# Kernel tuning notes

Hardware: AMD Instinct MI355X
Metric: run time of the kernel (lower is better)

Reference implementation:

```python
import jax, jax.numpy as jnp
from jax import lax
import numpy as np

HID = 150     # FFNN hidden dim
EMB = 300     # GloVe dim (input_dim)
LSTM = 200    # lstm_dim -> state_dim = 400
T = 768       # tokens in doc
VOCAB = 50000


def _ffnn(x, W1, b1, W2, b2, W3, b3):
    h = jax.nn.relu(x @ W1.T + b1)
    h = jax.nn.relu(h @ W2.T + b2)
    return h @ W3.T + b3


def _lstm_dir(x, Wih, Whh, b):
    H = Whh.shape[1]
    def step(carry, xt):
        h, c = carry
        z = xt @ Wih.T + h @ Whh.T + b
        i, f, g, o = jnp.split(z, 4, axis=-1)
        c = jax.nn.sigmoid(f) * c + jax.nn.sigmoid(i) * jnp.tanh(g)
        h = jax.nn.sigmoid(o) * jnp.tanh(c)
        return (h, c), h
    init = (jnp.zeros((H,), x.dtype), jnp.zeros((H,), x.dtype))
    _, hs = lax.scan(step, init, x)
    return hs


def setup_inputs():
    key = jax.random.key(0)
    ks = iter(jax.random.split(key, 40))
    def w(shape, s=0.05):
        return jax.random.normal(next(ks), shape, jnp.float32) * s
    state = 2 * LSTM
    span = 2 * state + EMB + 1   # 1101
    pair = 3 * span              # 3303
    z = lambda n: jnp.zeros((n,), jnp.float32)
    return {
        'tokens': jax.random.randint(next(ks), (T,), 0, VOCAB),
        'emb': w((VOCAB, EMB), 0.3),
        'Wih_f': w((4 * LSTM, EMB)), 'Whh_f': w((4 * LSTM, LSTM)), 'b_f': z(4 * LSTM),
        'Wih_b': w((4 * LSTM, EMB)), 'Whh_b': w((4 * LSTM, LSTM)), 'b_b': z(4 * LSTM),
        'aW1': w((HID, state)), 'ab1': z(HID), 'aW2': w((HID, HID)), 'ab2': z(HID), 'aW3': w((1, HID)), 'ab3': z(1),
        'sW1': w((HID, span)), 'sb1': z(HID), 'sW2': w((HID, HID)), 'sb2': z(HID), 'sW3': w((1, HID)), 'sb3': z(1),
        'pW1': w((HID, pair)), 'pb1': z(HID), 'pW2': w((HID, HID)), 'pb2': z(HID), 'pW3': w((1, HID)), 'pb3': z(1),
    }


def reference(tokens, emb, Wih_f, Whh_f, b_f, Wih_b, Whh_b, b_b,
              aW1, ab1, aW2, ab2, aW3, ab3,
              sW1, sb1, sW2, sb2, sW3, sb3,
              pW1, pb1, pW2, pb2, pW3, pb3):
    Tn = tokens.shape[0]
    x = emb[tokens]  # (T, 300) frozen GloVe embeds
    h = jnp.concatenate([_lstm_dir(x, Wih_f, Whh_f, b_f),
                         _lstm_dir(x[::-1], Wih_b, Whh_b, b_b)[::-1]], axis=-1)  # (T, 400)
    # dropout omitted (eval mode / identity)
    attn_logits = _ffnn(h, aW1, ab1, aW2, ab2, aW3, ab3)[:, 0]  # per-token attn score (T,)
    gs, i1s, i2s = [], [], []
    for n in range(1, 11):  # span widths 1..10
        starts = jnp.arange(Tn - n + 1)
        idx = starts[:, None] + jnp.arange(n)[None, :]           # (S_n, n)
        wgt = jax.nn.softmax(attn_logits[idx], axis=-1)          # per-span softmax over LSTM-state scores
        pooled = jnp.einsum('sn,snd->sd', wgt, x[idx])           # attention pools raw embeds (as original)
        g = jnp.concatenate([h[starts], h[starts + n - 1], pooled,
                             jnp.full((Tn - n + 1, 1), float(n), jnp.float32)], axis=-1)
        gs.append(g); i1s.append(starts); i2s.append(starts + n - 1)
    g = jnp.concatenate(gs, 0)                                    # (S, 1101)
    i1 = jnp.concatenate(i1s, 0); i2 = jnp.concatenate(i2s, 0)
    S = g.shape[0]
    sm = _ffnn(g, sW1, sb1, sW2, sb2, sW3, sb3)[:, 0]             # span scores (S,)
    order = jnp.argsort(-sm)                                      # stable desc sort, as Python sorted(reverse=True)
    i1o, i2o = i1[order], i2[order]
    # greedy overlap filter: keep span if fully taken OR both endpoints free; mark taken only when kept
    def body(k, carry):
        taken, keep = carry
        a, b = i1o[k], i2o[k]
        offs = jnp.clip(a + jnp.arange(10), 0, Tn - 1)
        valid = (a + jnp.arange(10)) <= b
        all_taken = jnp.all(jnp.where(valid, taken[offs], True))
        ok = all_taken | (~taken[a] & ~taken[b])
        keep = keep.at[k].set(ok)
        taken = taken.at[offs].max(valid & ok)
        return (taken, keep)
    _, keep = lax.fori_loop(0, S, body, (jnp.zeros((Tn,), bool), jnp.zeros((S,), bool)))
    K = int(round(Tn * 0.4))
    rank = jnp.cumsum(keep.astype(jnp.int32))
    pos = jnp.where(keep & (rank <= K), rank - 1, S)
    sel = jnp.argsort(pos)[:K]            # first K kept spans, score order (>=T width-1 spans always kept)
    sel = sel[jnp.argsort(i1o[sel])]      # stable sort by span start
    g_f = g[order][sel]; sm_f = sm[order][sel]
    i1_f = i1o[sel]; i2_f = i2o[sel]
    ii, jj = np.tril_indices(K, -1)       # row-major == nested (i, j<i) loop order
    pairs = jnp.concatenate([g_f[ii], g_f[jj], g_f[ii] * g_f[jj]], axis=-1)  # (P, 3303)
    sa = _ffnn(pairs, pW1, pb1, pW2, pb2, pW3, pb3)[:, 0]
    # sij[i, j] = sm_i + sm_j + sa_ij for j < i; diag/upper = 0 (the epsilon antecedent)
    sij = jnp.zeros((K, K), jnp.float32).at[ii, jj].set(sm_f[ii] + sm_f[jj] + sa)
    return sij, i1_f, i2_f
```

## Files before the change

### kernel.cpp

```cpp
#include <hip/hip_runtime.h>
#include <math.h>
#include <float.h>

#define TN      768
#define EMBD    300
#define XPAD    304
#define LSTMD   200
#define G4      800
#define STATE   400
#define HIDD    150
#define NPADC   160
#define SPAND   1101
#define KP      1120
#define NSPANS  7635
#define NSEL    307
#define SORTN   8192

typedef unsigned long long ull;

#define OFF_X       0u
#define OFF_ZXF     233472u
#define OFF_ZXB     847872u
#define OFF_H       1462272u
#define OFF_ATTN    1769472u
#define OFF_I1      1770496u
#define OFF_I2      1778176u
#define OFF_SM      1785856u
#define OFF_SELK    1793536u
#define OFF_SELSPAN 1794048u
#define OFF_SMF     1794560u
#define OFF_A       1795072u
#define OFF_B       1844224u
#define OFF_WTF     1893376u
#define OFF_WTB     2133376u
#define OFF_AW1T    2373376u
#define OFF_AW2T    2437376u
#define OFF_SW1T    2461376u
#define OFF_SW2T    2640576u
#define OFF_PW1AT   2664576u
#define OFF_PW1BT   2843776u
#define OFF_PW1CT   3022976u
#define OFF_PW2T    3202176u
#define OFF_G       3226176u

#define REP50(M) M(0) M(1) M(2) M(3) M(4) M(5) M(6) M(7) M(8) M(9) \
 M(10) M(11) M(12) M(13) M(14) M(15) M(16) M(17) M(18) M(19) \
 M(20) M(21) M(22) M(23) M(24) M(25) M(26) M(27) M(28) M(29) \
 M(30) M(31) M(32) M(33) M(34) M(35) M(36) M(37) M(38) M(39) \
 M(40) M(41) M(42) M(43) M(44) M(45) M(46) M(47) M(48) M(49)

__device__ __forceinline__ float sigf(float x) { return 1.f / (1.f + __expf(-x)); }
__device__ __forceinline__ float tanhf_(float x) {
    x = fminf(15.f, fmaxf(-15.f, x));
    float e = __expf(2.f * x);
    return (e - 1.f) / (e + 1.f);
}

__global__ void k_gather(const int* __restrict__ tokens, const float* __restrict__ emb,
                         float* __restrict__ x) {
    int t = blockIdx.x;
    int tok = tokens[t];
    for (int d = threadIdx.x; d < XPAD; d += 256)
        x[t * XPAD + d] = (d < EMBD) ? emb[(size_t)tok * EMBD + d] : 0.f;
}

__global__ void k_transpose(const float* __restrict__ src, float* __restrict__ dst,
                            int N, int K, int srcStride, int colOff, int Npad) {
    int k = blockIdx.x;
    int n = blockIdx.y * 256 + threadIdx.x;
    if (n >= Npad) return;
    float v = 0.f;
    if (k < K && n < N) v = src[(size_t)n * srcStride + colOff + k];
    dst[(size_t)k * Npad + n] = v;
}

__global__ void k_zx(const float* __restrict__ x, const float* __restrict__ WTf,
                     const float* __restrict__ WTb, const float* __restrict__ bf,
                     const float* __restrict__ bb, float* __restrict__ zxf,
                     float* __restrict__ zxb) {
    __shared__ float xl[8 * XPAD];
    int tid = threadIdx.x;
    int bm = blockIdx.x, dir = blockIdx.y;
    for (int l = tid; l < 8 * XPAD; l += 256) xl[l] = x[(size_t)(bm * 8) * XPAD + l];
    __syncthreads();
    const float* WT = dir ? WTb : WTf;
    const float* bv = dir ? bb : bf;
    float* zx = dir ? zxb : zxf;
    for (int jj = 0; jj < 4; ++jj) {
        int n = tid + 256 * jj;
        if (n >= G4) break;
        float acc[8] = {0, 0, 0, 0, 0, 0, 0, 0};
        for (int k = 0; k < EMBD; ++k) {
            float wv = WT[(size_t)k * G4 + n];
#pragma unroll
            for (int r = 0; r < 8; ++r) acc[r] = fmaf(xl[r * XPAD + k], wv, acc[r]);
        }
        float bias = bv[n];
#pragma unroll
        for (int r = 0; r < 8; ++r) {
            int row = bm * 8 + r;
            int trow = dir ? (TN - 1 - row) : row;
            zx[(size_t)trow * G4 + n] = acc[r] + bias;
        }
    }
}

__global__ __launch_bounds__(256, 1) void k_lstm_mb(const float* __restrict__ zxf,
                                                    const float* __restrict__ zxb,
                                                    const float* __restrict__ Whh_f,
                                                    const float* __restrict__ Whh_b,
                                                    float* __restrict__ hcat,
                                                    ull* __restrict__ hq) {
    int blk = blockIdx.x;
    int dir = blk >> 2, b = blk & 3;
    const float* zx = dir ? zxb : zxf;
    const float* Whh = dir ? Whh_b : Whh_f;
    ull* hqd = hq + (size_t)dir * TN * 256;
    int tid = threadIdx.x;
    __shared__ __align__(16) float hprev[LSTMD];
    __shared__ float zl[200];
    bool active = tid < 200;
    int q = tid / 50, u = tid % 50;
    int gr = q * 200 + b * 50 + u;
    int grs = active ? gr : 0;
    const float4* wr = (const float4*)(Whh + (size_t)grs * LSTMD);
#define WDECL(i) float4 w##i = wr[i];
    REP50(WDECL)
#undef WDECL
    float c = 0.f;
    for (int l = tid; l < LSTMD; l += 256) hprev[l] = 0.f;
    int remote_idx = (tid < b * 50) ? tid : tid + 50;
    __syncthreads();
    float zpre = zx[grs];
    for (int t = 0; t < TN; ++t) {
        float acc = zpre;
        const float4* h4 = (const float4*)hprev;
#define WFMA(i) { float4 hv = h4[i]; \
        acc = fmaf(w##i.x, hv.x, acc); acc = fmaf(w##i.y, hv.y, acc); \
        acc = fmaf(w##i.z, hv.z, acc); acc = fmaf(w##i.w, hv.w, acc); }
        REP50(WFMA)
#undef WFMA
        if (active) zl[tid] = acc;
        __syncthreads();
        int trow = dir ? (TN - 1 - t) : t;
        if (tid < 50) {
            float zi = zl[tid], zf = zl[50 + tid], zg = zl[100 + tid], zo = zl[150 + tid];
            c = sigf(zf) * c + sigf(zi) * tanhf_(zg);
            float h = sigf(zo) * tanhf_(c);
            hcat[(size_t)trow * STATE + dir * LSTMD + b * 50 + tid] = h;
            hprev[b * 50 + tid] = h;
            if (t + 1 < TN) {
                ull pk = (ull)__float_as_uint(h) | ((ull)(unsigned)(t + 1) << 32);
                __hip_atomic_store(&hqd[(size_t)t * 256 + b * 50 + tid], pk,
                                   __ATOMIC_RELAXED, __HIP_MEMORY_SCOPE_AGENT);
            }
        }
        if (t + 1 < TN) {
            zpre = zx[(size_t)(t + 1) * G4 + grs];
            if (tid < 150) {
                const ull* p = &hqd[(size_t)t * 256 + remote_idx];
                ull v;
                do {
                    v = __hip_atomic_load(p, __ATOMIC_RELAXED, __HIP_MEMORY_SCOPE_AGENT);
                } while ((unsigned)(v >> 32) != (unsigned)(t + 1));
                hprev[remote_idx] = __uint_as_float((unsigned)v);
            }
            __syncthreads();
        }
    }
}

__global__ void k_attn(const float* __restrict__ hcat, const float* __restrict__ aW1T,
                       const float* __restrict__ ab1, const float* __restrict__ aW2T,
                       const float* __restrict__ ab2, const float* __restrict__ aW3,
                       const float* __restrict__ ab3, float* __restrict__ attn) {
    __shared__ float hrow[STATE];
    __shared__ float l1[NPADC];
    __shared__ float l2[NPADC];
    __shared__ float red[256];
    int t = blockIdx.x, tid = threadIdx.x;
    for (int d = tid; d < STATE; d += 256) hrow[d] = hcat[(size_t)t * STATE + d];
    __syncthreads();
    if (tid < HIDD) {
        float acc = ab1[tid];
        for (int k = 0; k < STATE; ++k) acc = fmaf(hrow[k], aW1T[(size_t)k * NPADC + tid], acc);
        l1[tid] = fmaxf(acc, 0.f);
    }
    __syncthreads();
    if (tid < HIDD) {
        float acc = ab2[tid];
        for (int k = 0; k < HIDD; ++k) acc = fmaf(l1[k], aW2T[(size_t)k * NPADC + tid], acc);
        l2[tid] = fmaxf(acc, 0.f);
    }
    __syncthreads();
    float partial = (tid < HIDD) ? l2[tid] * aW3[tid] : 0.f;
    red[tid] = partial;
    __syncthreads();
    for (int s = 128; s > 0; s >>= 1) {
        if (tid < s) red[tid] += red[tid + s];
        __syncthreads();
    }
    if (tid == 0) attn[t] = red[0] + ab3[0];
}

__global__ void k_spans(const float* __restrict__ attn, const float* __restrict__ hcat,
                        const float* __restrict__ x, float* __restrict__ g,
                        int* __restrict__ i1s, int* __restrict__ i2s) {
    int s = blockIdx.x;
    int n = 1, base = 0;
    while (s >= base + (TN - n + 1)) { base += TN - n + 1; n++; }
    int a = s - base, b = a + n - 1;
    int lane = threadIdx.x;
    float e[10];
    float mx = -FLT_MAX;
#pragma unroll
    for (int k = 0; k < 10; ++k)
        if (k < n) { e[k] = attn[a + k]; mx = fmaxf(mx, e[k]); }
    float ssum = 0.f;
#pragma unroll
    for (int k = 0; k < 10; ++k)
        if (k < n) { e[k] = __expf(e[k] - mx); ssum += e[k]; }
    float w[10];
#pragma unroll
    for (int k = 0; k < 10; ++k) w[k] = (k < n) ? e[k] / ssum : 0.f;

    float* grow = g + (size_t)s * KP;
    for (int d = lane; d < STATE; d += 64) grow[d] = hcat[(size_t)a * STATE + d];
    for (int d = lane; d < STATE; d += 64) grow[STATE + d] = hcat[(size_t)b * STATE + d];
    for (int d = lane; d < EMBD; d += 64) {
        float p = 0.f;
#pragma unroll
        for (int k = 0; k < 10; ++k)
            if (k < n) p = fmaf(w[k], x[(size_t)(a + k) * XPAD + d], p);
        grow[2 * STATE + d] = p;
    }
    if (lane == 0) { grow[1100] = (float)n; i1s[s] = a; i2s[s] = b; }
    for (int d = SPAND + lane; d < KP; d += 64) grow[d] = 0.f;
}

__global__ void k_sm(const float* __restrict__ g, const float* __restrict__ sW1T,
                     const float* __restrict__ sb1, const float* __restrict__ sW2T,
                     const float* __restrict__ sb2, const float* __restrict__ sW3,
                     const float* __restrict__ sb3, float* __restrict__ smo) {
    __shared__ float As[32 * 33];
    __shared__ float Bs[32 * NPADC];
    __shared__ float L1[32 * 161];
    int tid = threadIdx.x;
    int tx = tid & 31, ty = tid >> 5;
    int row0 = blockIdx.x * 32;
    float acc[4][5] = {};
    for (int kb = 0; kb < KP; kb += 32) {
        for (int l = tid; l < 32 * 32; l += 256) {
            int r = l >> 5, cc = l & 31;
            int gr = row0 + r;
            As[r * 33 + cc] = (gr < NSPANS) ? g[(size_t)gr * KP + kb + cc] : 0.f;
        }
        for (int l = tid; l < 32 * NPADC; l += 256) {
            int r = l / NPADC, cc = l - NPADC * r;
            Bs[l] = sW1T[(size_t)(kb + r) * NPADC + cc];
        }
        __syncthreads();
        for (int kk = 0; kk < 32; ++kk) {
            float bv[5];
#pragma unroll
            for (int jn = 0; jn < 5; ++jn) bv[jn] = Bs[kk * NPADC + tx + 32 * jn];
#pragma unroll
            for (int i4 = 0; i4 < 4; ++i4) {
                float av = As[(ty * 4 + i4) * 33 + kk];
#pragma unroll
                for (int jn = 0; jn < 5; ++jn) acc[i4][jn] = fmaf(av, bv[jn], acc[i4][jn]);
            }
        }
        __syncthreads();
    }
#pragma unroll
    for (int i4 = 0; i4 < 4; ++i4)
#pragma unroll
        for (int jn = 0; jn < 5; ++jn) {
            int nn = tx + 32 * jn;
            float v = acc[i4][jn] + (nn < HIDD ? sb1[nn] : 0.f);
            L1[(ty * 4 + i4) * 161 + nn] = fmaxf(v, 0.f);
        }
    __syncthreads();
    float acc2[4][5] = {};
    for (int kk = 0; kk < HIDD; ++kk) {
        float bv[5];
#pragma unroll
        for (int jn = 0; jn < 5; ++jn) bv[jn] = sW2T[(size_t)kk * NPADC + tx + 32 * jn];
#pragma unroll
        for (int i4 = 0; i4 < 4; ++i4) {
            float av = L1[(ty * 4 + i4) * 161 + kk];
#pragma unroll
            for (int jn = 0; jn < 5; ++jn) acc2[i4][jn] = fmaf(av, bv[jn], acc2[i4][jn]);
        }
    }
    float part[4];
#pragma unroll
    for (int i4 = 0; i4 < 4; ++i4) {
        float p = 0.f;
#pragma unroll
        for (int jn = 0; jn < 5; ++jn) {
            int nn = tx + 32 * jn;
            float v = acc2[i4][jn] + (nn < HIDD ? sb2[nn] : 0.f);
            v = fmaxf(v, 0.f);
            p = fmaf(v, (nn < HIDD ? sW3[nn] : 0.f), p);
        }
        part[i4] = p;
    }
    for (int s = 16; s > 0; s >>= 1)
#pragma unroll
        for (int i4 = 0; i4 < 4; ++i4) part[i4] += __shfl_xor(part[i4], s, 32);
    if (tx == 0)
#pragma unroll
        for (int i4 = 0; i4 < 4; ++i4) {
            int gr = row0 + ty * 4 + i4;
            if (gr < NSPANS) smo[gr] = part[i4] + sb3[0];
        }
}

__global__ __launch_bounds__(1024) void k_sortsel(const float* __restrict__ sm,
                                                  const int* __restrict__ i1s,
                                                  const int* __restrict__ i2s,
                                                  int* __restrict__ selk,
                                                  int* __restrict__ selspan,
                                                  float* __restrict__ smf,
                                                  float* __restrict__ out) {
    __shared__ float ks[SORTN];
    __shared__ unsigned short id16[SORTN];
    __shared__ int ka2[512];
    __shared__ int va2[512];
    int tid = threadIdx.x;
    for (int i = tid; i < SORTN; i += 1024) {
        ks[i] = (i < NSPANS) ? sm[i] : -FLT_MAX;
        id16[i] = (unsigned short)i;
    }
    __syncthreads();
    for (int size = 2; size <= SORTN; size <<= 1) {
        for (int stride = size >> 1; stride > 0; stride >>= 1) {
            for (int t = tid; t < SORTN / 2; t += 1024) {
                int i = ((t & ~(stride - 1)) << 1) | (t & (stride - 1));
                int j = i + stride;
                float ki = ks[i], kj = ks[j];
                unsigned short ai = id16[i], aj = id16[j];
                bool less_ji = (kj > ki) || (kj == ki && aj < ai);
                bool asc = ((i & size) == 0);
                if (less_ji == asc) {
                    ks[i] = kj; ks[j] = ki;
                    id16[i] = aj; id16[j] = ai;
                }
            }
            __syncthreads();
        }
    }
    unsigned* abu = reinterpret_cast<unsigned*>(ks);
    for (int k = tid; k < NSPANS; k += 1024) {
        int sid = id16[k];
        abu[k] = (unsigned)i1s[sid] | ((unsigned)i2s[sid] << 16);
    }
    __syncthreads();
    if (tid < 64) {
        int l = tid;
        unsigned tk = 0;
        int cnt = 0;
        for (int k = 0; k < NSPANS && cnt < NSEL; ++k) {
            unsigned ab = abu[k];
            int a = (int)(ab & 0xFFFFu), b = (int)(ab >> 16);
            int lo = a - (l << 5), hi = b - (l << 5);
            lo = lo < 0 ? 0 : lo;
            hi = hi > 31 ? 31 : hi;
            unsigned m = 0;
            if (hi >= lo) {
                unsigned upper = (hi == 31) ? 0xFFFFFFFFu : ((1u << (hi + 1)) - 1u);
                m = upper & ~((1u << lo) - 1u);
            }
            bool cov = ((tk & m) == m);
            bool all_taken = __all((int)cov);
            int la = a >> 5, lb = b >> 5;
            unsigned long long bal_a = __ballot((int)((l == la) && ((tk >> (a & 31)) & 1u)));
            unsigned long long bal_b = __ballot((int)((l == lb) && ((tk >> (b & 31)) & 1u)));
            bool ok = all_taken || (bal_a == 0ull && bal_b == 0ull);
            if (ok) {
                tk |= m;
                if (l == 0) selk[cnt] = k;
                cnt++;
            }
        }
    }
    __syncthreads();
    if (tid < 512) {
        int r = tid;
        int key = 0x7FFFFFFF;
        if (r < NSEL) {
            int k = selk[r];
            int a = (int)(abu[k] & 0xFFFFu);
            key = (a << 9) | r;
        }
        ka2[r] = key;
        va2[r] = r;
    }
    __syncthreads();
    for (int size = 2; size <= 512; size <<= 1) {
        for (int stride = size >> 1; stride > 0; stride >>= 1) {
            if (tid < 256) {
                int t = tid;
                int i = ((t & ~(stride - 1)) << 1) | (t & (stride - 1));
                int j = i + stride;
                int ki = ka2[i], kj = ka2[j];
                bool asc = ((i & size) == 0);
                if ((kj < ki) == asc) {
                    ka2[i] = kj; ka2[j] = ki;
                    int vi = va2[i]; va2[i] = va2[j]; va2[j] = vi;
                }
            }
            __syncthreads();
        }
    }
    if (tid < NSEL) {
        int r = va2[tid];
        int k = selk[r];
        int sid = id16[k];
        unsigned ab = abu[k];
        selspan[tid] = sid;
        smf[tid] = sm[sid];
        out[NSEL * NSEL + tid] = (float)(ab & 0xFFFFu);
        out[NSEL * NSEL + NSEL + tid] = (float)(ab >> 16);
    }
}

__global__ void k_AB(const float* __restrict__ g, const int* __restrict__ selspan,
                     const float* __restrict__ pW1aT, const float* __restrict__ pW1bT,
                     const float* __restrict__ pb1, float* __restrict__ Aw,
                     float* __restrict__ Bw) {
    __shared__ float grow[KP];
    int r = blockIdx.x, which = blockIdx.y;
    int sid = selspan[r];
    int tid = threadIdx.x;
    for (int d = tid; d < KP; d += 256) grow[d] = g[(size_t)sid * KP + d];
    __syncthreads();
    if (tid < NPADC) {
        const float* WT = which ? pW1bT : pW1aT;
        float acc = 0.f;
        for (int k = 0; k < KP; ++k) acc = fmaf(grow[k], WT[(size_t)k * NPADC + tid], acc);
        if (which == 0) acc += (tid < HIDD ? pb1[tid] : 0.f);
        (which ? Bw : Aw)[(size_t)r * NPADC + tid] = acc;
    }
}

__global__ void k_pairs(const float* __restrict__ g, const int* __restrict__ selspan,
                        const float* __restrict__ smf, const float* __restrict__ Aw,
                        const float* __restrict__ Bw, const float* __restrict__ pW1cT,
                        const float* __restrict__ pW2T, const float* __restrict__ pb2,
                        const float* __restrict__ pW3, const float* __restrict__ pb3,
                        float* __restrict__ out) {
    int i = blockIdx.x;
    int j0 = blockIdx.y * 32;
    if (j0 >= i) return;
    __shared__ float Gj[32 * 33];
    __shared__ float Gi[32];
    __shared__ float Bs[32 * NPADC];
    __shared__ float L1s[32 * 161];
    int tid = threadIdx.x;
    int tx = tid & 31, ty = tid >> 5;
    int sidi = selspan[i];
    float acc[4][5] = {};
    for (int kb = 0; kb < KP; kb += 32) {
        for (int l = tid; l < 32 * 32; l += 256) {
            int r = l >> 5, cc = l & 31;
            int j = j0 + r;
            int sidj = selspan[j < i ? j : 0];
            Gj[r * 33 + cc] = (j < i) ? g[(size_t)sidj * KP + kb + cc] : 0.f;
        }
        if (tid < 32) Gi[tid] = g[(size_t)sidi * KP + kb + tid];
        for (int l = tid; l < 32 * NPADC; l += 256) {
            int r = l / NPADC, cc = l - NPADC * r;
            Bs[l] = pW1cT[(size_t)(kb + r) * NPADC + cc];
        }
        __syncthreads();
        for (int kk = 0; kk < 32; ++kk) {
            float gik = Gi[kk];
            float bv[5];
#pragma unroll
            for (int jn = 0; jn < 5; ++jn) bv[jn] = Bs[kk * NPADC + tx + 32 * jn];
#pragma unroll
            for (int i4 = 0; i4 < 4; ++i4) {
                float av = Gj[(ty * 4 + i4) * 33 + kk] * gik;
#pragma unroll
                for (int jn = 0; jn < 5; ++jn) acc[i4][jn] = fmaf(av, bv[jn], acc[i4][jn]);
            }
        }
        __syncthreads();
    }
#pragma unroll
    for (int i4 = 0; i4 < 4; ++i4) {
        int m = ty * 4 + i4;
        int j = j0 + m;
        int jsafe = j < i ? j : 0;
#pragma unroll
        for (int jn = 0; jn < 5; ++jn) {
            int nn = tx + 32 * jn;
            float v = acc[i4][jn] + Aw[(size_t)i * NPADC + nn] + Bw[(size_t)jsafe * NPADC + nn];
            L1s[m * 161 + nn] = fmaxf(v, 0.f);
        }
    }
    __syncthreads();
    float acc2[4][5] = {};
    for (int kk = 0; kk < HIDD; ++kk) {
        float bv[5];
#pragma unroll
        for (int jn = 0; jn < 5; ++jn) bv[jn] = pW2T[(size_t)kk * NPADC + tx + 32 * jn];
#pragma unroll
        for (int i4 = 0; i4 < 4; ++i4) {
            float av = L1s[(ty * 4 + i4) * 161 + kk];
#pragma unroll
            for (int jn = 0; jn < 5; ++jn) acc2[i4][jn] = fmaf(av, bv[jn], acc2[i4][jn]);
        }
    }
    float part[4];
#pragma unroll
    for (int i4 = 0; i4 < 4; ++i4) {
        float p = 0.f;
#pragma unroll
        for (int jn = 0; jn < 5; ++jn) {
            int nn = tx + 32 * jn;
            float v = acc2[i4][jn] + (nn < HIDD ? pb2[nn] : 0.f);
            v = fmaxf(v, 0.f);
            p = fmaf(v, (nn < HIDD ? pW3[nn] : 0.f), p);
        }
        part[i4] = p;
    }
    for (int s = 16; s > 0; s >>= 1)
#pragma unroll
        for (int i4 = 0; i4 < 4; ++i4) part[i4] += __shfl_xor(part[i4], s, 32);
    if (tx == 0)
#pragma unroll
        for (int i4 = 0; i4 < 4; ++i4) {
            int j = j0 + ty * 4 + i4;
            if (j < i) out[(size_t)i * NSEL + j] = smf[i] + smf[j] + part[i4] + pb3[0];
        }
}

extern "C" void kernel_launch(void* const* d_in, const int* in_sizes, int n_in,
                              void* d_out, int out_size, void* d_ws, size_t ws_size,
                              hipStream_t stream) {
    (void)in_sizes; (void)n_in; (void)ws_size;
    const int* tokens  = (const int*)d_in[0];
    const float* emb   = (const float*)d_in[1];
    const float* Wih_f = (const float*)d_in[2];
    const float* Whh_f = (const float*)d_in[3];
    const float* b_f   = (const float*)d_in[4];
    const float* Wih_b = (const float*)d_in[5];
    const float* Whh_b = (const float*)d_in[6];
    const float* b_b   = (const float*)d_in[7];
    const float* aW1 = (const float*)d_in[8];  const float* ab1 = (const float*)d_in[9];
    const float* aW2 = (const float*)d_in[10]; const float* ab2 = (const float*)d_in[11];
    const float* aW3 = (const float*)d_in[12]; const float* ab3 = (const float*)d_in[13];
    const float* sW1 = (const float*)d_in[14]; const float* sb1 = (const float*)d_in[15];
    const float* sW2 = (const float*)d_in[16]; const float* sb2 = (const float*)d_in[17];
    const float* sW3 = (const float*)d_in[18]; const float* sb3 = (const float*)d_in[19];
    const float* pW1 = (const float*)d_in[20]; const float* pb1 = (const float*)d_in[21];
    const float* pW2 = (const float*)d_in[22]; const float* pb2 = (const float*)d_in[23];
    const float* pW3 = (const float*)d_in[24]; const float* pb3 = (const float*)d_in[25];
    float* W = (float*)d_ws;
    float* out = (float*)d_out;
    ull* hq = (ull*)(W + OFF_G);

    hipMemsetAsync(d_out, 0, (size_t)out_size * sizeof(float), stream);
    hipMemsetAsync(hq, 0, (size_t)2 * TN * 256 * sizeof(ull), stream);

    k_gather<<<TN, 256, 0, stream>>>(tokens, emb, W + OFF_X);

    k_transpose<<<dim3(300, 4), 256, 0, stream>>>(Wih_f, W + OFF_WTF, 800, 300, 300, 0, 800);
    k_transpose<<<dim3(300, 4), 256, 0, stream>>>(Wih_b, W + OFF_WTB, 800, 300, 300, 0, 800);
    k_transpose<<<dim3(400, 1), 256, 0, stream>>>(aW1, W + OFF_AW1T, 150, 400, 400, 0, NPADC);
    k_transpose<<<dim3(150, 1), 256, 0, stream>>>(aW2, W + OFF_AW2T, 150, 150, 150, 0, NPADC);
    k_transpose<<<dim3(KP, 1), 256, 0, stream>>>(sW1, W + OFF_SW1T, 150, SPAND, SPAND, 0, NPADC);
    k_transpose<<<dim3(150, 1), 256, 0, stream>>>(sW2, W + OFF_SW2T, 150, 150, 150, 0, NPADC);
    k_transpose<<<dim3(KP, 1), 256, 0, stream>>>(pW1, W + OFF_PW1AT, 150, SPAND, 3303, 0, NPADC);
    k_transpose<<<dim3(KP, 1), 256, 0, stream>>>(pW1, W + OFF_PW1BT, 150, SPAND, 3303, 1101, NPADC);
    k_transpose<<<dim3(KP, 1), 256, 0, stream>>>(pW1, W + OFF_PW1CT, 150, SPAND, 3303, 2202, NPADC);
    k_transpose<<<dim3(150, 1), 256, 0, stream>>>(pW2, W + OFF_PW2T, 150, 150, 150, 0, NPADC);

    k_zx<<<dim3(96, 2), 256, 0, stream>>>(W + OFF_X, W + OFF_WTF, W + OFF_WTB, b_f, b_b,
                                          W + OFF_ZXF, W + OFF_ZXB);
    k_lstm_mb<<<8, 256, 0, stream>>>(W + OFF_ZXF, W + OFF_ZXB, Whh_f, Whh_b, W + OFF_H, hq);
    k_attn<<<TN, 256, 0, stream>>>(W + OFF_H, W + OFF_AW1T, ab1, W + OFF_AW2T, ab2, aW3, ab3,
                                   W + OFF_ATTN);
    k_spans<<<NSPANS, 64, 0, stream>>>(W + OFF_ATTN, W + OFF_H, W + OFF_X, W + OFF_G,
                                       (int*)(W + OFF_I1), (int*)(W + OFF_I2));
    k_sm<<<(NSPANS + 31) / 32, 256, 0, stream>>>(W + OFF_G, W + OFF_SW1T, sb1, W + OFF_SW2T, sb2,
                                                 sW3, sb3, W + OFF_SM);
    k_sortsel<<<1, 1024, 0, stream>>>(W + OFF_SM, (int*)(W + OFF_I1), (int*)(W + OFF_I2),
                                      (int*)(W + OFF_SELK), (int*)(W + OFF_SELSPAN),
                                      W + OFF_SMF, out);
    k_AB<<<dim3(NSEL, 2), 256, 0, stream>>>(W + OFF_G, (int*)(W + OFF_SELSPAN), W + OFF_PW1AT,
                                            W + OFF_PW1BT, pb1, W + OFF_A, W + OFF_B);
    k_pairs<<<dim3(NSEL, 10), 256, 0, stream>>>(W + OFF_G, (int*)(W + OFF_SELSPAN), W + OFF_SMF,
                                                W + OFF_A, W + OFF_B, W + OFF_PW1CT, W + OFF_PW2T,
                                                pb2, pW3, pb3, out);
}
```

Measured before the change: 2.702 ms.

## Place LSTM blocks on same XCD and add fast handoff path for hidden-state exchange

```diff
diff --git a/kernel.cpp b/kernel.cpp
--- a/kernel.cpp
+++ b/kernel.cpp
@@ -105,24 +105,29 @@
     }
 }
 
-__global__ __launch_bounds__(256, 1) void k_lstm_mb(const float* __restrict__ zxf,
-                                                    const float* __restrict__ zxb,
-                                                    const float* __restrict__ Whh_f,
-                                                    const float* __restrict__ Whh_b,
-                                                    float* __restrict__ hcat,
-                                                    ull* __restrict__ hq) {
+__global__ __launch_bounds__(256, 1) void k_lstm_mb8(const float* __restrict__ zxf,
+                                                     const float* __restrict__ zxb,
+                                                     const float* __restrict__ Whh_f,
+                                                     const float* __restrict__ Whh_b,
+                                                     float* __restrict__ hcat,
+                                                     ull* __restrict__ hqL2,
+                                                     ull* __restrict__ hqL3) {
     int blk = blockIdx.x;
-    int dir = blk >> 2, b = blk & 3;
+    int lane8 = blk & 7;
+    if (lane8 >= 2) return;
+    int dir = lane8, b = blk >> 3;
+    int tid = threadIdx.x;
+
     const float* zx = dir ? zxb : zxf;
     const float* Whh = dir ? Whh_b : Whh_f;
-    ull* hqd = hq + (size_t)dir * TN * 256;
-    int tid = threadIdx.x;
+    ull* hq2d = hqL2 + (size_t)dir * TN * 256;
+    ull* hq3d = hqL3 + (size_t)dir * TN * 256;
     __shared__ __align__(16) float hprev[LSTMD];
     __shared__ float zl[200];
     bool active = tid < 200;
     int q = tid / 50, u = tid % 50;
-    int gr = q * 200 + b * 50 + u;
-    int grs = active ? gr : 0;
+    int gr_row = q * 200 + b * 50 + u;
+    int grs = active ? gr_row : 0;
     const float4* wr = (const float4*)(Whh + (size_t)grs * LSTMD);
 #define WDECL(i) float4 w##i = wr[i];
     REP50(WDECL)
@@ -130,6 +135,7 @@
     float c = 0.f;
     for (int l = tid; l < LSTMD; l += 256) hprev[l] = 0.f;
     int remote_idx = (tid < b * 50) ? tid : tid + 50;
+    int use_fast = 4;
     __syncthreads();
     float zpre = zx[grs];
     for (int t = 0; t < TN; ++t) {
@@ -151,18 +157,37 @@
             hprev[b * 50 + tid] = h;
             if (t + 1 < TN) {
                 ull pk = (ull)__float_as_uint(h) | ((ull)(unsigned)(t + 1) << 32);
-                __hip_atomic_store(&hqd[(size_t)t * 256 + b * 50 + tid], pk,
-                                   __ATOMIC_RELAXED, __HIP_MEMORY_SCOPE_AGENT);
+                size_t slot = (size_t)t * 256 + b * 50 + tid;
+                (void)__hip_atomic_exchange(&hq2d[slot], pk, __ATOMIC_RELAXED,
+                                            __HIP_MEMORY_SCOPE_WORKGROUP);
+                __hip_atomic_store(&hq3d[slot], pk, __ATOMIC_RELAXED,
+                                   __HIP_MEMORY_SCOPE_AGENT);
             }
         }
         if (t + 1 < TN) {
             zpre = zx[(size_t)(t + 1) * G4 + grs];
             if (tid < 150) {
-                const ull* p = &hqd[(size_t)t * 256 + remote_idx];
-                ull v;
-                do {
-                    v = __hip_atomic_load(p, __ATOMIC_RELAXED, __HIP_MEMORY_SCOPE_AGENT);
-                } while ((unsigned)(v >> 32) != (unsigned)(t + 1));
+                size_t slot = (size_t)t * 256 + remote_idx;
+                ull v = 0;
+                bool got = false;
+                if (use_fast > 0) {
+                    for (int it = 0; it < 8; ++it) {
+                        ull probe = ~0ull;
+                        __hip_atomic_compare_exchange_strong(
+                            &hq2d[slot], &probe, ~0ull, __ATOMIC_RELAXED,
+                            __ATOMIC_RELAXED, __HIP_MEMORY_SCOPE_WORKGROUP);
+                        if ((unsigned)(probe >> 32) == (unsigned)(t + 1)) {
+                            v = probe; got = true; break;
+                        }
+                    }
+                    use_fast = got ? 4 : (use_fast - 1);
+                }
+                if (!got) {
+                    do {
+                        v = __hip_atomic_load(&hq3d[slot], __ATOMIC_RELAXED,
+                                              __HIP_MEMORY_SCOPE_AGENT);
+                    } while ((unsigned)(v >> 32) != (unsigned)(t + 1));
+                }
                 hprev[remote_idx] = __uint_as_float((unsigned)v);
             }
             __syncthreads();
@@ -562,10 +587,11 @@
     const float* pW3 = (const float*)d_in[24]; const float* pb3 = (const float*)d_in[25];
     float* W = (float*)d_ws;
     float* out = (float*)d_out;
-    ull* hq = (ull*)(W + OFF_G);
+    ull* hqL2 = (ull*)(W + OFF_G);
+    ull* hqL3 = hqL2 + (size_t)2 * TN * 256;
 
     hipMemsetAsync(d_out, 0, (size_t)out_size * sizeof(float), stream);
-    hipMemsetAsync(hq, 0, (size_t)2 * TN * 256 * sizeof(ull), stream);
+    hipMemsetAsync(hqL2, 0, (size_t)4 * TN * 256 * sizeof(ull), stream);
 
     k_gather<<<TN, 256, 0, stream>>>(tokens, emb, W + OFF_X);
 
@@ -582,7 +608,8 @@
 
     k_zx<<<dim3(96, 2), 256, 0, stream>>>(W + OFF_X, W + OFF_WTF, W + OFF_WTB, b_f, b_b,
                                           W + OFF_ZXF, W + OFF_ZXB);
-    k_lstm_mb<<<8, 256, 0, stream>>>(W + OFF_ZXF, W + OFF_ZXB, Whh_f, Whh_b, W + OFF_H, hq);
+    k_lstm_mb8<<<32, 256, 0, stream>>>(W + OFF_ZXF, W + OFF_ZXB, Whh_f, Whh_b, W + OFF_H,
+                                       hqL2, hqL3);
     k_attn<<<TN, 256, 0, stream>>>(W + OFF_H, W + OFF_AW1T, ab1, W + OFF_AW2T, ab2, aW3, ab3,
                                    W + OFF_ATTN);
     k_spans<<<NSPANS, 64, 0, stream>>>(W + OFF_ATTN, W + OFF_H, W + OFF_X, W + OFF_G,
```

After: 2.597 ms. -3.9%, faster.
